# Performance work log

Measured on AMD Instinct MI355X. Metric: run time of the kernel, lower is better.

Reference implementation:

```python
import jax, jax.numpy as jnp
from jax import lax
import numpy as np

NUM_BINS = 4
GROUPS = 196
PS = 16  # patch_size
CH = 3 * GROUPS  # 588


def quick_gelu(x):
    return x * jax.nn.sigmoid(1.702 * x)


def avgpool3_exclude_pad(x):
    # AvgPool2d(kernel=3, stride=1, padding=1, count_include_pad=False)
    win = (1, 1, 3, 3)
    strides = (1, 1, 1, 1)
    pad = ((0, 0), (0, 0), (1, 1), (1, 1))
    s = lax.reduce_window(x, jnp.float32(0.0), lax.add, win, strides, pad)
    ones = jnp.ones((1, 1) + x.shape[-2:], x.dtype)
    cnt = lax.reduce_window(ones, jnp.float32(0.0), lax.add, win, strides, pad)
    return s / cnt


def setup_inputs() -> dict:
    key = jax.random.key(0)
    ks = jax.random.split(key, 6)
    B = 64
    x = jax.random.normal(ks[0], (B, 197, 768), jnp.float32)
    # adapter_conv: Conv2d(588,588,3,groups=196) -> OIHW weight [588,3,3,3]
    conv_w = jax.random.normal(ks[1], (CH, 3, 3, 3), jnp.float32) * (1.0 / np.sqrt(27.0))
    conv_b = jnp.zeros((CH,), jnp.float32)
    # HistogramLayer: bin_centers_conv.bias (learnable), bin_widths_conv.weight (learnable)
    centers = jax.random.normal(ks[2], (NUM_BINS * CH,), jnp.float32) * 0.1
    widths = jax.random.normal(ks[3], (NUM_BINS * CH,), jnp.float32) * 0.1 + 1.0
    # adapter_conv_down: Conv2d(2352,588,1,groups=196) -> per-group [3 out, 12 in]
    down_w = jax.random.normal(ks[4], (GROUPS, 3, 12), jnp.float32) * 0.1
    down_b = jax.random.normal(ks[5], (CH,), jnp.float32) * 0.1
    return dict(x=x, conv_w=conv_w, conv_b=conv_b, centers=centers,
                widths=widths, down_w=down_w, down_b=down_b)


def reference(x, conv_w, conv_b, centers, widths, down_w, down_b):
    B, N, C = x.shape  # (64, 197, 768)
    x_cls = x[:, :1, :]
    xp = x[:, 1:, :].reshape(B, (N - 1) * 3, PS, PS)  # (B, 588, 16, 16)

    # grouped 3x3 conv, groups=196 (3->3 per group)
    y = lax.conv_general_dilated(
        xp, conv_w, window_strides=(1, 1), padding=((1, 1), (1, 1)),
        dimension_numbers=('NCHW', 'OIHW', 'NCHW'), feature_group_count=GROUPS)
    y = y + conv_b[None, :, None, None]
    y = quick_gelu(y)

    # HistogramLayer: bin_centers (weight frozen at 1) -> abs; bin_widths (bias frozen at 1) -> relu
    h = jnp.abs(jnp.repeat(y, NUM_BINS, axis=1) + centers[None, :, None, None])  # (B, 2352, 16, 16)
    h = jax.nn.relu(widths[None, :, None, None] * h + 1.0)

    # constrain_bins: per-(channel-group of 4 bins) sum-normalize
    Bn, Cn, H, W = h.shape
    hr = h.reshape(Bn, Cn // NUM_BINS, NUM_BINS, H, W)
    h = (hr / (hr.sum(axis=2, keepdims=True) + 1e-5)).reshape(Bn, Cn, H, W)

    # normalize_count: AvgPool2d(3, stride=1, pad=1, count_include_pad=False)
    h = avgpool3_exclude_pad(h)
    h = quick_gelu(h)

    # adapter_conv_down: grouped 1x1 conv, 12 -> 3 per group of 196
    hg = h.reshape(B, GROUPS, 12, H, W)
    o = jnp.einsum('bgihw,goi->bgohw', hg, down_w) + down_b.reshape(1, GROUPS, 3, 1, 1)
    o = o.reshape(B, GROUPS, 768)  # (3*16*16 = 768 per patch token)

    return jnp.concatenate([x_cls, o], axis=1)  # (B, 197, 768)
```

## Files before the change

kernel.cpp:

```cpp
#include <hip/hip_runtime.h>

#define GROUPS 196

__device__ __forceinline__ float dppL(float v) {
    return __int_as_float(__builtin_amdgcn_update_dpp(
        __float_as_int(v), __float_as_int(v), 0x111, 0xF, 0xF, true));
}
__device__ __forceinline__ float dppR(float v) {
    return __int_as_float(__builtin_amdgcn_update_dpp(
        __float_as_int(v), __float_as_int(v), 0x101, 0xF, 0xF, true));
}
__device__ __forceinline__ float qgelu(float v) {
    return v * __builtin_amdgcn_rcpf(1.0f + __expf(-1.702f * v));
}
__device__ __forceinline__ float qgelu01(float p) {
    float s = fmaf(p, 0.041056f, -0.126448f);
    s = fmaf(p, s, 0.006306f);
    s = fmaf(p, s, 0.424881f);
    s = fmaf(p, s, 0.5f);
    return p * s;
}

#define LDS_FENCE() asm volatile("s_waitcnt lgkmcnt(0)" ::: "memory")
#define F4C(v, j) ((j) == 0 ? (v).x : (j) == 1 ? (v).y : (j) == 2 ? (v).z : (v).w)

__global__ __launch_bounds__(256) void convpass_fused(
    const float* __restrict__ x,
    const float* __restrict__ conv_w,
    const float* __restrict__ conv_b,
    const float* __restrict__ centers,
    const float* __restrict__ widths,
    const float* __restrict__ down_w,
    const float* __restrict__ down_b,
    float* __restrict__ out)
{
    const int tid = threadIdx.x;
    const int l  = tid & 63;
    const int wv = tid >> 6;
    const int g  = blockIdx.x * 4 + wv;
    const int b  = blockIdx.y;
    const int py = l >> 2;
    const int q  = l & 3;
    const bool q0 = (q == 0), q3 = (q == 3);
    const float mL = q0 ? 0.f : 1.f;
    const float mR = q3 ? 0.f : 1.f;

    __shared__ float4 sIN[4][3][18][4];
    __shared__ float4 sRS[4][3][18][4];

    const int sg = __builtin_amdgcn_readfirstlane(g);
    const float* cw  = conv_w  + sg * 81;
    const float* cen = centers + sg * 12;
    const float* wid = widths  + sg * 12;
    const float* dwp = down_w  + sg * 36;
    const float cb0 = conv_b[sg*3+0], cb1 = conv_b[sg*3+1], cb2 = conv_b[sg*3+2];
    const float db0 = down_b[sg*3+0], db1 = down_b[sg*3+1], db2 = down_b[sg*3+2];

    const int tok = b * 197 + g + 1;
    const float4* xin4 = (const float4*)x + tok * 192;
    const float4 A0 = xin4[l];
    const float4 A1 = xin4[64 + l];
    const float4 A2 = xin4[128 + l];

    if (l < 24) {
        const int ic = l >> 3, rem = l & 7;
        const int row = (rem >> 2) ? 17 : 0;
        const int col = rem & 3;
        const float4 z = make_float4(0.f, 0.f, 0.f, 0.f);
        sIN[wv][ic][row][col] = z;
        sRS[wv][ic][row][col] = z;
    }
    sIN[wv][0][py + 1][q] = A0;
    sIN[wv][1][py + 1][q] = A1;
    sIN[wv][2][py + 1][q] = A2;

    LDS_FENCE();

    float4 V[3][3];
    V[0][1] = A0; V[1][1] = A1; V[2][1] = A2;
    #pragma unroll
    for (int ic = 0; ic < 3; ++ic) {
        V[ic][0] = sIN[wv][ic][py][q];
        V[ic][2] = sIN[wv][ic][py + 2][q];
    }

    float L[3][3], R[3][3];
    #pragma unroll
    for (int ic = 0; ic < 3; ++ic) {
        #pragma unroll
        for (int r = 0; r < 3; ++r) {
            L[ic][r] = dppL(V[ic][r].w) * mL;
            R[ic][r] = dppR(V[ic][r].x) * mR;
        }
    }

    float acc[3][4];
    #pragma unroll
    for (int j = 0; j < 4; ++j) { acc[0][j] = cb0; acc[1][j] = cb1; acc[2][j] = cb2; }
    #pragma unroll
    for (int oc = 0; oc < 3; ++oc) {
        #pragma unroll
        for (int ic = 0; ic < 3; ++ic) {
            #pragma unroll
            for (int r = 0; r < 3; ++r) {
                const float w0 = cw[oc*27 + ic*9 + r*3 + 0];
                const float w1 = cw[oc*27 + ic*9 + r*3 + 1];
                const float w2 = cw[oc*27 + ic*9 + r*3 + 2];
                const float4 v = V[ic][r];
                acc[oc][0] = fmaf(L[ic][r], w0, fmaf(v.x, w1, fmaf(v.y, w2, acc[oc][0])));
                acc[oc][1] = fmaf(v.x,      w0, fmaf(v.y, w1, fmaf(v.z, w2, acc[oc][1])));
                acc[oc][2] = fmaf(v.y,      w0, fmaf(v.z, w1, fmaf(v.w, w2, acc[oc][2])));
                acc[oc][3] = fmaf(v.z,      w0, fmaf(v.w, w1, fmaf(R[ic][r], w2, acc[oc][3])));
            }
        }
    }

    float yv[3][4];
    #pragma unroll
    for (int oc = 0; oc < 3; ++oc)
        #pragma unroll
        for (int j = 0; j < 4; ++j)
            yv[oc][j] = qgelu(acc[oc][j]);

    const bool  vy2 = (py == 0) | (py == 15);
    const float rEdge = vy2 ? 0.25f     : (1.f/6.f);
    const float rMid  = vy2 ? (1.f/6.f) : (1.f/9.f);
    const float rc[4] = { q0 ? rEdge : rMid, rMid, rMid, q3 ? rEdge : rMid };

    float o[3][4];
    #pragma unroll
    for (int j = 0; j < 4; ++j) { o[0][j] = db0; o[1][j] = db1; o[2][j] = db2; }

    #pragma unroll
    for (int oc = 0; oc < 3; ++oc) {
        float hj[3][4];
        #pragma unroll
        for (int j = 0; j < 4; ++j) {
            const float y = yv[oc][j];
            const float t0 = fmaf(wid[oc*4+0], fabsf(y + cen[oc*4+0]), 1.0f);
            const float t1 = fmaf(wid[oc*4+1], fabsf(y + cen[oc*4+1]), 1.0f);
            const float t2 = fmaf(wid[oc*4+2], fabsf(y + cen[oc*4+2]), 1.0f);
            const float t3 = fmaf(wid[oc*4+3], fabsf(y + cen[oc*4+3]), 1.0f);
            const float inv = __builtin_amdgcn_rcpf((t0 + t1) + (t2 + t3));
            hj[0][j] = t0 * inv; hj[1][j] = t1 * inv; hj[2][j] = t2 * inv;
        }
        float rs[3][4];
        #pragma unroll
        for (int k = 0; k < 3; ++k) {
            const float lh = dppL(hj[k][3]) * mL;
            const float rh = dppR(hj[k][0]) * mR;
            const float s01 = hj[k][0] + hj[k][1];
            const float s23 = hj[k][2] + hj[k][3];
            rs[k][0] = lh + s01;
            rs[k][1] = s01 + hj[k][2];
            rs[k][2] = hj[k][1] + s23;
            rs[k][3] = s23 + rh;
        }

        LDS_FENCE();
        #pragma unroll
        for (int k = 0; k < 3; ++k)
            sRS[wv][k][py + 1][q] = make_float4(rs[k][0], rs[k][1], rs[k][2], rs[k][3]);
        LDS_FENCE();

        float4 up[3], dn[3];
        #pragma unroll
        for (int k = 0; k < 3; ++k) {
            up[k] = sRS[wv][k][py][q];
            dn[k] = sRS[wv][k][py + 2][q];
        }

        #pragma unroll
        for (int j = 0; j < 4; ++j) {
            const float p0 = (rs[0][j] + F4C(up[0], j) + F4C(dn[0], j)) * rc[j];
            const float p1 = (rs[1][j] + F4C(up[1], j) + F4C(dn[1], j)) * rc[j];
            const float p2 = (rs[2][j] + F4C(up[2], j) + F4C(dn[2], j)) * rc[j];
            const float p3 = 1.0f - p0 - p1 - p2;
            const float u0 = qgelu01(p0);
            const float u1 = qgelu01(p1);
            const float u2 = qgelu01(p2);
            const float u3 = qgelu01(p3);
            const int i = oc * 4;
            o[0][j] = fmaf(u0, dwp[i],    fmaf(u1, dwp[i+1],    fmaf(u2, dwp[i+2],    fmaf(u3, dwp[i+3],    o[0][j]))));
            o[1][j] = fmaf(u0, dwp[12+i], fmaf(u1, dwp[12+i+1], fmaf(u2, dwp[12+i+2], fmaf(u3, dwp[12+i+3], o[1][j]))));
            o[2][j] = fmaf(u0, dwp[24+i], fmaf(u1, dwp[24+i+1], fmaf(u2, dwp[24+i+2], fmaf(u3, dwp[24+i+3], o[2][j]))));
        }
    }

    float4* op4 = (float4*)out + tok * 192;
    op4[l]       = make_float4(o[0][0], o[0][1], o[0][2], o[0][3]);
    op4[64 + l]  = make_float4(o[1][0], o[1][1], o[1][2], o[1][3]);
    op4[128 + l] = make_float4(o[2][0], o[2][1], o[2][2], o[2][3]);

    if (g == 0) {
        const float4* xc = (const float4*)x + b * 197 * 192;
        float4* oc4 = (float4*)out + b * 197 * 192;
        oc4[l]       = xc[l];
        oc4[64 + l]  = xc[64 + l];
        oc4[128 + l] = xc[128 + l];
    }
}

extern "C" void kernel_launch(void* const* d_in, const int* in_sizes, int n_in,
                              void* d_out, int out_size, void* d_ws, size_t ws_size,
                              hipStream_t stream) {
    const float* x       = (const float*)d_in[0];
    const float* conv_w  = (const float*)d_in[1];
    const float* conv_b  = (const float*)d_in[2];
    const float* centers = (const float*)d_in[3];
    const float* widths  = (const float*)d_in[4];
    const float* down_w  = (const float*)d_in[5];
    const float* down_b  = (const float*)d_in[6];
    float* out = (float*)d_out;

    const int B = in_sizes[0] / (197 * 768);

    dim3 grid(GROUPS / 4, B);
    convpass_fused<<<grid, 256, 0, stream>>>(x, conv_w, conv_b, centers, widths,
                                             down_w, down_b, out);
}
```

Before: 30.60 us.

## Remap lanes row-major within DPP rows and replace LDS halo exchange with DPP/bpermute

Lanes are remapped so that each 16-lane DPP row holds one column quarter, with the 16 image rows spread across its lanes. Vertical neighbours then come from row_shr/row_shl DPP with zero-fill at the row ends, and horizontal neighbours across quarters come from ds_bpermute. This removes the LDS staging buffers, their zero-padding writes and the lgkmcnt fences in both the conv input halo and the avgpool vertical sum. The cost is many more DPP ops, bpermute traffic (which still goes through the LDS crossbar), and strided global float4 loads and stores instead of contiguous per-lane addresses.

```diff
diff --git a/kernel.cpp b/kernel.cpp
--- a/kernel.cpp
+++ b/kernel.cpp
@@ -9,6 +9,9 @@
 __device__ __forceinline__ float dppR(float v) {
     return __int_as_float(__builtin_amdgcn_update_dpp(
         __float_as_int(v), __float_as_int(v), 0x101, 0xF, 0xF, true));
+}
+__device__ __forceinline__ float bperm(int addr, float v) {
+    return __int_as_float(__builtin_amdgcn_ds_bpermute(addr, __float_as_int(v)));
 }
 __device__ __forceinline__ float qgelu(float v) {
     return v * __builtin_amdgcn_rcpf(1.0f + __expf(-1.702f * v));
@@ -20,9 +23,6 @@
     s = fmaf(p, s, 0.5f);
     return p * s;
 }
-
-#define LDS_FENCE() asm volatile("s_waitcnt lgkmcnt(0)" ::: "memory")
-#define F4C(v, j) ((j) == 0 ? (v).x : (j) == 1 ? (v).y : (j) == 2 ? (v).z : (v).w)
 
 __global__ __launch_bounds__(256) void convpass_fused(
     const float* __restrict__ x,
@@ -39,14 +39,12 @@
     const int wv = tid >> 6;
     const int g  = blockIdx.x * 4 + wv;
     const int b  = blockIdx.y;
-    const int py = l >> 2;
-    const int q  = l & 3;
-    const bool q0 = (q == 0), q3 = (q == 3);
-    const float mL = q0 ? 0.f : 1.f;
-    const float mR = q3 ? 0.f : 1.f;
-
-    __shared__ float4 sIN[4][3][18][4];
-    __shared__ float4 sRS[4][3][18][4];
+    const int q  = l >> 4;
+    const int py = l & 15;
+    const float mL = (q > 0) ? 1.f : 0.f;
+    const float mR = (q < 3) ? 1.f : 0.f;
+    const int aL = ((l - 16) & 63) << 2;
+    const int aR = ((l + 16) & 63) << 2;
 
     const int sg = __builtin_amdgcn_readfirstlane(g);
     const float* cw  = conv_w  + sg * 81;
@@ -58,30 +56,18 @@
 
     const int tok = b * 197 + g + 1;
     const float4* xin4 = (const float4*)x + tok * 192;
-    const float4 A0 = xin4[l];
-    const float4 A1 = xin4[64 + l];
-    const float4 A2 = xin4[128 + l];
-
-    if (l < 24) {
-        const int ic = l >> 3, rem = l & 7;
-        const int row = (rem >> 2) ? 17 : 0;
-        const int col = rem & 3;
-        const float4 z = make_float4(0.f, 0.f, 0.f, 0.f);
-        sIN[wv][ic][row][col] = z;
-        sRS[wv][ic][row][col] = z;
-    }
-    sIN[wv][0][py + 1][q] = A0;
-    sIN[wv][1][py + 1][q] = A1;
-    sIN[wv][2][py + 1][q] = A2;
-
-    LDS_FENCE();
+    const int fo = py * 4 + q;
+    const float4 A0 = xin4[fo];
+    const float4 A1 = xin4[64 + fo];
+    const float4 A2 = xin4[128 + fo];
 
     float4 V[3][3];
     V[0][1] = A0; V[1][1] = A1; V[2][1] = A2;
     #pragma unroll
     for (int ic = 0; ic < 3; ++ic) {
-        V[ic][0] = sIN[wv][ic][py][q];
-        V[ic][2] = sIN[wv][ic][py + 2][q];
+        const float4 a = V[ic][1];
+        V[ic][0] = make_float4(dppL(a.x), dppL(a.y), dppL(a.z), dppL(a.w));
+        V[ic][2] = make_float4(dppR(a.x), dppR(a.y), dppR(a.z), dppR(a.w));
     }
 
     float L[3][3], R[3][3];
@@ -89,8 +75,8 @@
     for (int ic = 0; ic < 3; ++ic) {
         #pragma unroll
         for (int r = 0; r < 3; ++r) {
-            L[ic][r] = dppL(V[ic][r].w) * mL;
-            R[ic][r] = dppR(V[ic][r].x) * mR;
+            L[ic][r] = bperm(aL, V[ic][r].w) * mL;
+            R[ic][r] = bperm(aR, V[ic][r].x) * mR;
         }
     }
 
@@ -123,9 +109,9 @@
             yv[oc][j] = qgelu(acc[oc][j]);
 
     const bool  vy2 = (py == 0) | (py == 15);
-    const float rEdge = vy2 ? 0.25f     : (1.f/6.f);
-    const float rMid  = vy2 ? (1.f/6.f) : (1.f/9.f);
-    const float rc[4] = { q0 ? rEdge : rMid, rMid, rMid, q3 ? rEdge : rMid };
+    const float rE = vy2 ? 0.25f     : (1.f/6.f);
+    const float rM = vy2 ? (1.f/6.f) : (1.f/9.f);
+    const float rc[4] = { (q == 0) ? rE : rM, rM, rM, (q == 3) ? rE : rM };
 
     float o[3][4];
     #pragma unroll
@@ -147,34 +133,27 @@
         float rs[3][4];
         #pragma unroll
         for (int k = 0; k < 3; ++k) {
-            const float lh = dppL(hj[k][3]) * mL;
-            const float rh = dppR(hj[k][0]) * mR;
+            const float lh = bperm(aL, hj[k][3]);
+            const float rh = bperm(aR, hj[k][0]);
             const float s01 = hj[k][0] + hj[k][1];
             const float s23 = hj[k][2] + hj[k][3];
-            rs[k][0] = lh + s01;
+            rs[k][0] = fmaf(mL, lh, s01);
             rs[k][1] = s01 + hj[k][2];
             rs[k][2] = hj[k][1] + s23;
-            rs[k][3] = s23 + rh;
-        }
-
-        LDS_FENCE();
-        #pragma unroll
-        for (int k = 0; k < 3; ++k)
-            sRS[wv][k][py + 1][q] = make_float4(rs[k][0], rs[k][1], rs[k][2], rs[k][3]);
-        LDS_FENCE();
-
-        float4 up[3], dn[3];
+            rs[k][3] = fmaf(mR, rh, s23);
+        }
+        float vs[3][4];
         #pragma unroll
         for (int k = 0; k < 3; ++k) {
-            up[k] = sRS[wv][k][py][q];
-            dn[k] = sRS[wv][k][py + 2][q];
-        }
-
+            #pragma unroll
+            for (int j = 0; j < 4; ++j)
+                vs[k][j] = rs[k][j] + dppL(rs[k][j]) + dppR(rs[k][j]);
+        }
         #pragma unroll
         for (int j = 0; j < 4; ++j) {
-            const float p0 = (rs[0][j] + F4C(up[0], j) + F4C(dn[0], j)) * rc[j];
-            const float p1 = (rs[1][j] + F4C(up[1], j) + F4C(dn[1], j)) * rc[j];
-            const float p2 = (rs[2][j] + F4C(up[2], j) + F4C(dn[2], j)) * rc[j];
+            const float p0 = vs[0][j] * rc[j];
+            const float p1 = vs[1][j] * rc[j];
+            const float p2 = vs[2][j] * rc[j];
             const float p3 = 1.0f - p0 - p1 - p2;
             const float u0 = qgelu01(p0);
             const float u1 = qgelu01(p1);
@@ -188,9 +167,9 @@
     }
 
     float4* op4 = (float4*)out + tok * 192;
-    op4[l]       = make_float4(o[0][0], o[0][1], o[0][2], o[0][3]);
-    op4[64 + l]  = make_float4(o[1][0], o[1][1], o[1][2], o[1][3]);
-    op4[128 + l] = make_float4(o[2][0], o[2][1], o[2][2], o[2][3]);
+    op4[fo]       = make_float4(o[0][0], o[0][1], o[0][2], o[0][3]);
+    op4[64 + fo]  = make_float4(o[1][0], o[1][1], o[1][2], o[1][3]);
+    op4[128 + fo] = make_float4(o[2][0], o[2][1], o[2][2], o[2][3]);
 
     if (g == 0) {
         const float4* xc = (const float4*)x + b * 197 * 192;
```

Result: slower. 31.90 us (+4.3%).
